# Optimization experiments

Measured on AMD Instinct MI355X. Metric: run time of the kernel, lower is better.

## Reference

```python
import jax, jax.numpy as jnp
import numpy as np

N, E, D, H = 50000, 800000, 256, 256
EPS = 1e-12


def _sage_pool(h, src, dst, W_pool, b_pool, W_self, W_neigh, b):
    # DGL SAGEConv aggregator_type='pool':
    #   m = relu(fc_pool(h_src)); h_neigh = max over in-neighbors; 
    #   out = fc_self(h_dst) + fc_neigh(h_neigh) + bias
    m = jax.nn.relu(h @ W_pool + b_pool)                # [N, D]
    msgs = m[src]                                        # [E, D] irregular gather
    agg = jax.ops.segment_max(msgs, dst, num_segments=N)  # [N, D]
    agg = jnp.where(jnp.isfinite(agg), agg, 0.0)         # zero-in-degree -> 0
    return h @ W_self + agg @ W_neigh + b


def _l2norm(h):
    # torch F.normalize(dim=1)
    n = jnp.linalg.norm(h, axis=1, keepdims=True)
    return h / jnp.maximum(n, EPS)


def setup_inputs() -> dict:
    key = jax.random.key(0)
    ks = jax.random.split(key, 13)
    s = 1.0 / np.sqrt(D)
    inp = {
        "x": jax.random.normal(ks[0], (N, D), jnp.float32),
        "src": jax.random.randint(ks[1], (E,), 0, N, jnp.int32),
        "dst": jax.random.randint(ks[2], (E,), 0, N, jnp.int32),
        "W_pool0": jax.random.normal(ks[3], (D, D), jnp.float32) * s,
        "b_pool0": jnp.zeros((D,), jnp.float32),
        "W_self0": jax.random.normal(ks[4], (D, H), jnp.float32) * s,
        "W_neigh0": jax.random.normal(ks[5], (D, H), jnp.float32) * s,
        "b0": jnp.zeros((H,), jnp.float32),
        "W_pool1": jax.random.normal(ks[6], (H, H), jnp.float32) * s,
        "b_pool1": jnp.zeros((H,), jnp.float32),
        "W_self1": jax.random.normal(ks[7], (H, H), jnp.float32) * s,
        "W_neigh1": jax.random.normal(ks[8], (H, H), jnp.float32) * s,
        "b1": jnp.zeros((H,), jnp.float32),
    }
    return inp


def reference(x, src, dst, W_pool0, b_pool0, W_self0, W_neigh0, b0,
              W_pool1, b_pool1, W_self1, W_neigh1, b1):
    # layer 0: conv -> relu -> l2-normalize -> dropout (identity at eval)
    h = _sage_pool(x, src, dst, W_pool0, b_pool0, W_self0, W_neigh0, b0)
    h = _l2norm(jax.nn.relu(h))
    enc_feat_input = h
    # layer 1 (last): conv only
    h = _sage_pool(h, src, dst, W_pool1, b_pool1, W_self1, W_neigh1, b1)
    return (h, enc_feat_input)
```

## Files before the change

### kernel.cpp

```cpp
#include <hip/hip_runtime.h>
#include <cstddef>

#define D256 256

typedef __attribute__((ext_vector_type(8))) short bf16x8;
typedef __attribute__((ext_vector_type(4))) float f32x4;

#define GLOAD16(gptr, lptr)                                                         \
    __builtin_amdgcn_global_load_lds(                                               \
        (const __attribute__((address_space(1))) unsigned int*)(gptr),              \
        (__attribute__((address_space(3))) unsigned int*)(lptr), 16, 0, 0)

__device__ __forceinline__ ushort f2bf(float f) {
    unsigned u = __float_as_uint(f);
    return (ushort)((u + 0x7FFFu + ((u >> 16) & 1u)) >> 16);
}
__device__ __forceinline__ ushort umax16(ushort a, ushort b) { return a > b ? a : b; }
__device__ __forceinline__ ushort4 vmax4(ushort4 a, ushort4 b) {
    return make_ushort4(umax16(a.x, b.x), umax16(a.y, b.y),
                        umax16(a.z, b.z), umax16(a.w, b.w));
}

template<int DUAL, int RELU, int OUT_BF16>
__global__ __launch_bounds__(256)
void mfma_gemm_kernel(const ushort* __restrict__ A, const ushort* __restrict__ Bt,
                      const ushort* __restrict__ A2, const ushort* __restrict__ Bt2,
                      const float* __restrict__ bias, void* __restrict__ outp, int M)
{
    constexpr int TILES = DUAL ? 4 : 2;
    constexpr int BUFSZ = TILES * 4096;
    __shared__ ushort smem[2 * BUFSZ];

    const int nwg  = gridDim.x;
    const int q    = nwg >> 3, r = nwg & 7;
    const int xcd  = blockIdx.x & 7, jj = blockIdx.x >> 3;
    const int wgid = (xcd < r ? xcd * (q + 1) : r * (q + 1) + (xcd - r) * q) + jj;

    const int t    = threadIdx.x;
    const int m0   = (wgid >> 1) * 128;
    const int n0   = (wgid & 1) * 128;
    const int lane = t & 63;
    const int wave = t >> 6;
    const int wr   = (wave >> 1) * 64;
    const int wc   = (wave & 1) * 64;
    const int lr   = lane & 15;
    const int kg   = lane >> 4;

    const int lrow  = lane >> 2;
    const int lch   = lane & 3;
    const int srow0 = wave * 32;

    f32x4 acc[4][4];
#pragma unroll
    for (int i = 0; i < 4; ++i)
#pragma unroll
        for (int j = 0; j < 4; ++j) acc[i][j] = (f32x4)(0.0f);

    auto STAGE = [&](int buf, int k0) {
        ushort* const base = smem + buf * BUFSZ;
#pragma unroll
        for (int i = 0; i < 2; ++i) {
            const int r2  = srow0 + i * 16;
            const int ar  = m0 + r2 + lrow;
            const int arc = ar < M ? ar : (M - 1);
            const size_t ga = (size_t)arc * D256 + k0 + lch * 8;
            const size_t gb = (size_t)(n0 + r2 + lrow) * D256 + k0 + lch * 8;
            GLOAD16(A + ga, base + r2 * 32);
            GLOAD16(Bt + gb, base + 4096 + r2 * 32);
            if (DUAL) {
                GLOAD16(A2 + ga, base + 8192 + r2 * 32);
                GLOAD16(Bt2 + gb, base + 12288 + r2 * 32);
            }
        }
    };

    STAGE(0, 0);
#pragma unroll
    for (int ks = 0; ks < 8; ++ks) {
        const int cur = ks & 1;
        __syncthreads();
        if (ks < 7) STAGE(cur ^ 1, (ks + 1) * 32);

        ushort* const base = smem + cur * BUFSZ;
        bf16x8 af[4], bf[4];
#pragma unroll
        for (int mi = 0; mi < 4; ++mi)
            af[mi] = *(const bf16x8*)&base[(wr + mi * 16 + lr) * 32 + kg * 8];
#pragma unroll
        for (int ni = 0; ni < 4; ++ni)
            bf[ni] = *(const bf16x8*)&base[4096 + (wc + ni * 16 + lr) * 32 + kg * 8];
#pragma unroll
        for (int mi = 0; mi < 4; ++mi)
#pragma unroll
            for (int ni = 0; ni < 4; ++ni)
                acc[mi][ni] = __builtin_amdgcn_mfma_f32_16x16x32_bf16(
                    bf[ni], af[mi], acc[mi][ni], 0, 0, 0);
        if (DUAL) {
            bf16x8 af2[4], bf2[4];
#pragma unroll
            for (int mi = 0; mi < 4; ++mi)
                af2[mi] = *(const bf16x8*)&base[8192 + (wr + mi * 16 + lr) * 32 + kg * 8];
#pragma unroll
            for (int ni = 0; ni < 4; ++ni)
                bf2[ni] = *(const bf16x8*)&base[12288 + (wc + ni * 16 + lr) * 32 + kg * 8];
#pragma unroll
            for (int mi = 0; mi < 4; ++mi)
#pragma unroll
                for (int ni = 0; ni < 4; ++ni)
                    acc[mi][ni] = __builtin_amdgcn_mfma_f32_16x16x32_bf16(
                        bf2[ni], af2[mi], acc[mi][ni], 0, 0, 0);
        }
    }

#pragma unroll
    for (int ni = 0; ni < 4; ++ni) {
        const int colb = n0 + wc + ni * 16 + kg * 4;
        const float4 bb = *(const float4*)(bias + colb);
#pragma unroll
        for (int mi = 0; mi < 4; ++mi) {
            const int row = m0 + wr + mi * 16 + lr;
            if (row < M) {
                const f32x4 a = acc[mi][ni];
                float4 o;
                o.x = a[0] + bb.x;
                o.y = a[1] + bb.y;
                o.z = a[2] + bb.z;
                o.w = a[3] + bb.w;
                if (RELU) {
                    o.x = fmaxf(o.x, 0.f); o.y = fmaxf(o.y, 0.f);
                    o.z = fmaxf(o.z, 0.f); o.w = fmaxf(o.w, 0.f);
                }
                if (OUT_BF16) {
                    ushort4 ob;
                    ob.x = f2bf(o.x); ob.y = f2bf(o.y);
                    ob.z = f2bf(o.z); ob.w = f2bf(o.w);
                    *(ushort4*)((ushort*)outp + (size_t)row * D256 + colb) = ob;
                } else {
                    *(float4*)((float*)outp + (size_t)row * D256 + colb) = o;
                }
            }
        }
    }
}

__global__ __launch_bounds__(256)
void f2bf_kernel(const float* __restrict__ in, ushort* __restrict__ out, int n4)
{
    const int i = blockIdx.x * 256 + threadIdx.x;
    if (i >= n4) return;
    const float4 v = ((const float4*)in)[i];
    ushort4 o;
    o.x = f2bf(v.x); o.y = f2bf(v.y); o.z = f2bf(v.z); o.w = f2bf(v.w);
    ((ushort4*)out)[i] = o;
}

struct WP  { const float* w; ushort* o; };
struct WP6 { WP p[6]; };
__global__ __launch_bounds__(256)
void wtrans_kernel(WP6 ps)
{
    const float* __restrict__ W = ps.p[blockIdx.z].w;
    ushort* __restrict__ O      = ps.p[blockIdx.z].o;
    __shared__ float sm[32][33];
    const int tx = threadIdx.x & 31, ty = threadIdx.x >> 5;
    const int k0 = blockIdx.x * 32, n0 = blockIdx.y * 32;
#pragma unroll
    for (int i = 0; i < 4; ++i)
        sm[ty + i * 8][tx] = W[(size_t)(k0 + ty + i * 8) * D256 + n0 + tx];
    __syncthreads();
#pragma unroll
    for (int i = 0; i < 4; ++i)
        O[(size_t)(n0 + ty + i * 8) * D256 + k0 + tx] = f2bf(sm[tx][ty + i * 8]);
}

__global__ __launch_bounds__(256)
void hist_kernel(const int* __restrict__ dst, int* __restrict__ deg, int E)
{
    const int nq = E >> 2;
    const int i  = blockIdx.x * 256 + threadIdx.x;
    if (i < nq) {
        const int4 d = ((const int4*)dst)[i];
        atomicAdd(&deg[d.x], 1);
        atomicAdd(&deg[d.y], 1);
        atomicAdd(&deg[d.z], 1);
        atomicAdd(&deg[d.w], 1);
    } else if (i == nq) {
        for (int e = nq * 4; e < E; ++e) atomicAdd(&deg[dst[e]], 1);
    }
}

__global__ __launch_bounds__(1024)
void blockscan_kernel(const int* __restrict__ deg, int* __restrict__ incl,
                      int* __restrict__ partials, int N)
{
    __shared__ int wt[16];
    const int i    = blockIdx.x * 1024 + threadIdx.x;
    const int lane = threadIdx.x & 63;
    const int wv   = threadIdx.x >> 6;
    const int v    = (i < N) ? deg[i] : 0;
    int s = v;
#pragma unroll
    for (int o = 1; o < 64; o <<= 1) {
        const int t = __shfl_up(s, o);
        if (lane >= o) s += t;
    }
    if (lane == 63) wt[wv] = s;
    __syncthreads();
    if (wv == 0 && lane < 16) {
        const int w = wt[lane];
        int ws = w;
#pragma unroll
        for (int o = 1; o < 16; o <<= 1) {
            const int t = __shfl_up(ws, o);
            if (lane >= o) ws += t;
        }
        wt[lane] = ws - w;
    }
    __syncthreads();
    s += wt[wv];
    if (i < N) incl[i] = s;
    if (threadIdx.x == 1023) partials[blockIdx.x] = s;
}

__global__ __launch_bounds__(1024)
void scanp_kernel(int* __restrict__ partials, int nb)
{
    __shared__ int sm[1024];
    const int v = (threadIdx.x < (unsigned)nb) ? partials[threadIdx.x] : 0;
    sm[threadIdx.x] = v;
    __syncthreads();
#pragma unroll
    for (int off = 1; off < 1024; off <<= 1) {
        const int t = (threadIdx.x >= (unsigned)off) ? sm[threadIdx.x - off] : 0;
        __syncthreads();
        sm[threadIdx.x] += t;
        __syncthreads();
    }
    if (threadIdx.x < (unsigned)nb) partials[threadIdx.x] = sm[threadIdx.x] - v;
}

__global__ __launch_bounds__(1024)
void finalize_kernel(const int* __restrict__ deg, const int* __restrict__ incl,
                     const int* __restrict__ partials, int* __restrict__ row_ptr,
                     int* __restrict__ cursor, int N, int E)
{
    const int i = blockIdx.x * 1024 + threadIdx.x;
    if (i < N) {
        const int ex = partials[blockIdx.x] + incl[i] - deg[i];
        row_ptr[i] = ex;
        cursor[i]  = ex;
    }
    if (i == 0) row_ptr[N] = E;
}

__global__ __launch_bounds__(256)
void bucket_kernel(const int* __restrict__ src, const int* __restrict__ dst,
                   int* __restrict__ cursor, int* __restrict__ esrc, int E)
{
    const int nq = E >> 2;
    const int i  = blockIdx.x * 256 + threadIdx.x;
    if (i < nq) {
        const int4 d = ((const int4*)dst)[i];
        const int4 s = ((const int4*)src)[i];
        esrc[atomicAdd(&cursor[d.x], 1)] = s.x;
        esrc[atomicAdd(&cursor[d.y], 1)] = s.y;
        esrc[atomicAdd(&cursor[d.z], 1)] = s.z;
        esrc[atomicAdd(&cursor[d.w], 1)] = s.w;
    } else if (i == nq) {
        for (int e = nq * 4; e < E; ++e)
            esrc[atomicAdd(&cursor[dst[e]], 1)] = src[e];
    }
}

__global__ __launch_bounds__(256)
void agg_max_kernel(const int* __restrict__ row_ptr, const int* __restrict__ esrc,
                    const ushort* __restrict__ m, ushort* __restrict__ agg, int N)
{
    const int wid  = (int)(((size_t)blockIdx.x * 256 + threadIdx.x) >> 6);
    const int lane = threadIdx.x & 63;
    if (wid >= N) return;
    const int beg = row_ptr[wid];
    const int end = row_ptr[wid + 1];
    const size_t off = (size_t)(lane * 4);

    ushort4 a0 = make_ushort4(0, 0, 0, 0);
    ushort4 a1 = a0, a2 = a0, a3 = a0;
    int e = beg;
    for (; e + 8 <= end; e += 8) {
        int s[8];
#pragma unroll
        for (int q = 0; q < 8; ++q) s[q] = esrc[e + q];
        ushort4 v[8];
#pragma unroll
        for (int q = 0; q < 8; ++q)
            v[q] = *(const ushort4*)(m + (size_t)s[q] * D256 + off);
        a0 = vmax4(a0, vmax4(v[0], v[4]));
        a1 = vmax4(a1, vmax4(v[1], v[5]));
        a2 = vmax4(a2, vmax4(v[2], v[6]));
        a3 = vmax4(a3, vmax4(v[3], v[7]));
    }
    for (; e + 2 <= end; e += 2) {
        const int s0 = esrc[e];
        const int s1 = esrc[e + 1];
        const ushort4 v0 = *(const ushort4*)(m + (size_t)s0 * D256 + off);
        const ushort4 v1 = *(const ushort4*)(m + (size_t)s1 * D256 + off);
        a0 = vmax4(a0, v0);
        a1 = vmax4(a1, v1);
    }
    if (e < end) {
        const ushort4 v0 = *(const ushort4*)(m + (size_t)esrc[e] * D256 + off);
        a2 = vmax4(a2, v0);
    }
    const ushort4 r = vmax4(vmax4(a0, a1), vmax4(a2, a3));
    *(ushort4*)(agg + (size_t)wid * D256 + off) = r;
}

__global__ __launch_bounds__(256)
void l2norm_kernel(const float* __restrict__ in, float* __restrict__ out_f,
                   ushort* __restrict__ out_b, int M)
{
    const int wid  = (int)(((size_t)blockIdx.x * 256 + threadIdx.x) >> 6);
    const int lane = threadIdx.x & 63;
    if (wid >= M) return;
    const float4 v = *(const float4*)(in + (size_t)wid * D256 + lane * 4);
    float ss = v.x * v.x + v.y * v.y + v.z * v.z + v.w * v.w;
#pragma unroll
    for (int o = 32; o >= 1; o >>= 1) ss += __shfl_xor(ss, o);
    const float inv = 1.0f / fmaxf(sqrtf(ss), 1e-12f);
    float4 o4;
    o4.x = v.x * inv; o4.y = v.y * inv; o4.z = v.z * inv; o4.w = v.w * inv;
    *(float4*)(out_f + (size_t)wid * D256 + lane * 4) = o4;
    ushort4 ob;
    ob.x = f2bf(o4.x); ob.y = f2bf(o4.y); ob.z = f2bf(o4.z); ob.w = f2bf(o4.w);
    *(ushort4*)(out_b + (size_t)wid * D256 + lane * 4) = ob;
}

extern "C" void kernel_launch(void* const* d_in, const int* in_sizes, int n_in,
                              void* d_out, int out_size, void* d_ws, size_t ws_size,
                              hipStream_t stream)
{
    const float* x        = (const float*)d_in[0];
    const int*   src      = (const int*)  d_in[1];
    const int*   dst      = (const int*)  d_in[2];
    const float* W_pool0  = (const float*)d_in[3];
    const float* b_pool0  = (const float*)d_in[4];
    const float* W_self0  = (const float*)d_in[5];
    const float* W_neigh0 = (const float*)d_in[6];
    const float* b0       = (const float*)d_in[7];
    const float* W_pool1  = (const float*)d_in[8];
    const float* b_pool1  = (const float*)d_in[9];
    const float* W_self1  = (const float*)d_in[10];
    const float* W_neigh1 = (const float*)d_in[11];
    const float* b1       = (const float*)d_in[12];

    const int N = in_sizes[0] / D256;
    const int E = in_sizes[1];
    const size_t NR = (size_t)N * D256;

    float* h1  = (float*)d_out;
    float* enc = (float*)d_out + NR;

    ushort* xb   = (ushort*)d_ws;
    ushort* mb   = xb + NR;
    ushort* aggb = mb + NR;
    float*  tmp  = (float*)(aggb + NR);
    ushort* Bt   = (ushort*)(tmp + NR);
    int* row_ptr = (int*)(Bt + 6 * 256 * 256);
    int* cursor  = row_ptr + (N + 1);
    int* deg     = cursor + N;
    int* incl    = deg + N;
    int* partials= incl + N;
    int* esrc    = partials + 1024;

    ushort* Bt_pool0  = Bt + 0 * 65536;
    ushort* Bt_self0  = Bt + 1 * 65536;
    ushort* Bt_neigh0 = Bt + 2 * 65536;
    ushort* Bt_pool1  = Bt + 3 * 65536;
    ushort* Bt_self1  = Bt + 4 * 65536;
    ushort* Bt_neigh1 = Bt + 5 * 65536;

    const int  gemm_blocks = ((N + 127) / 128) * 2;
    const int  q_blocks    = ((E >> 2) + 1 + 255) / 256;
    const int  node_blocks = (N + 3) / 4;
    const int  conv_blocks = (int)((NR / 4 + 255) / 256);
    const int  scan_blocks = (N + 1023) / 1024;

    WP6 wp;
    wp.p[0] = { W_pool0,  Bt_pool0  };
    wp.p[1] = { W_self0,  Bt_self0  };
    wp.p[2] = { W_neigh0, Bt_neigh0 };
    wp.p[3] = { W_pool1,  Bt_pool1  };
    wp.p[4] = { W_self1,  Bt_self1  };
    wp.p[5] = { W_neigh1, Bt_neigh1 };
    wtrans_kernel<<<dim3(8, 8, 6), 256, 0, stream>>>(wp);
    f2bf_kernel<<<conv_blocks, 256, 0, stream>>>(x, xb, (int)(NR / 4));

    hipMemsetAsync(deg, 0, (size_t)N * sizeof(int), stream);
    hist_kernel<<<q_blocks, 256, 0, stream>>>(dst, deg, E);
    blockscan_kernel<<<scan_blocks, 1024, 0, stream>>>(deg, incl, partials, N);
    scanp_kernel<<<1, 1024, 0, stream>>>(partials, scan_blocks);
    finalize_kernel<<<scan_blocks, 1024, 0, stream>>>(deg, incl, partials,
                                                      row_ptr, cursor, N, E);
    bucket_kernel<<<q_blocks, 256, 0, stream>>>(src, dst, cursor, esrc, E);

    mfma_gemm_kernel<0,1,1><<<gemm_blocks, 256, 0, stream>>>(xb, Bt_pool0, nullptr, nullptr,
                                                             b_pool0, mb, N);
    agg_max_kernel<<<node_blocks, 256, 0, stream>>>(row_ptr, esrc, mb, aggb, N);
    mfma_gemm_kernel<1,1,0><<<gemm_blocks, 256, 0, stream>>>(xb, Bt_self0, aggb, Bt_neigh0,
                                                             b0, tmp, N);
    l2norm_kernel<<<node_blocks, 256, 0, stream>>>(tmp, enc, xb, N);

    mfma_gemm_kernel<0,1,1><<<gemm_blocks, 256, 0, stream>>>(xb, Bt_pool1, nullptr, nullptr,
                                                             b_pool1, mb, N);
    agg_max_kernel<<<node_blocks, 256, 0, stream>>>(row_ptr, esrc, mb, aggb, N);
    mfma_gemm_kernel<1,0,0><<<gemm_blocks, 256, 0, stream>>>(xb, Bt_self1, aggb, Bt_neigh1,
                                                             b1, h1, N);
}
```

Baseline: 357.4 us.

## Fuse layer-0 dual GEMM with ReLU and L2 normalization epilogue

After: 355.4 us. Within noise of the previous version (-0.6%).

```diff
diff --git a/kernel.cpp b/kernel.cpp
--- a/kernel.cpp
+++ b/kernel.cpp
@@ -144,6 +144,129 @@
 }
 
 __global__ __launch_bounds__(256)
+void mfma_dual_l2n_kernel(const ushort* A, const ushort* __restrict__ Bt,
+                          const ushort* __restrict__ A2, const ushort* __restrict__ Bt2,
+                          const float* __restrict__ bias,
+                          float* __restrict__ enc_f, ushort* enc_b, int M)
+{
+    __shared__ ushort smem[24576];
+    __shared__ float  ssq_lds[128][2];
+
+    const int t    = threadIdx.x;
+    const int m0   = blockIdx.x * 128;
+    const int lane = t & 63;
+    const int wave = t >> 6;
+    const int wr   = (wave >> 1) * 64;
+    const int wc   = (wave & 1) * 128;
+    const int lr   = lane & 15;
+    const int kg   = lane >> 4;
+    const int lrow = lane >> 2;
+    const int lch  = lane & 3;
+
+    f32x4 acc[4][8];
+#pragma unroll
+    for (int i = 0; i < 4; ++i)
+#pragma unroll
+        for (int j = 0; j < 8; ++j) acc[i][j] = (f32x4)(0.0f);
+
+    for (int ks = 0; ks < 8; ++ks) {
+        const int k0 = ks * 32;
+        __syncthreads();
+#pragma unroll
+        for (int i = 0; i < 2; ++i) {
+            const int r2  = wave * 32 + i * 16;
+            const int ar  = m0 + r2 + lrow;
+            const int arc = ar < M ? ar : (M - 1);
+            const size_t ga = (size_t)arc * D256 + k0 + lch * 8;
+            GLOAD16(A + ga, smem + r2 * 32);
+            GLOAD16(A2 + ga, smem + 12288 + r2 * 32);
+        }
+#pragma unroll
+        for (int i = 0; i < 4; ++i) {
+            const int r2 = wave * 64 + i * 16;
+            const size_t gb = (size_t)(r2 + lrow) * D256 + k0 + lch * 8;
+            GLOAD16(Bt + gb, smem + 4096 + r2 * 32);
+            GLOAD16(Bt2 + gb, smem + 16384 + r2 * 32);
+        }
+        __syncthreads();
+
+        bf16x8 af[4];
+#pragma unroll
+        for (int mi = 0; mi < 4; ++mi)
+            af[mi] = *(const bf16x8*)&smem[(wr + mi * 16 + lr) * 32 + kg * 8];
+#pragma unroll
+        for (int ni = 0; ni < 8; ++ni) {
+            const bf16x8 b = *(const bf16x8*)&smem[4096 + (wc + ni * 16 + lr) * 32 + kg * 8];
+#pragma unroll
+            for (int mi = 0; mi < 4; ++mi)
+                acc[mi][ni] = __builtin_amdgcn_mfma_f32_16x16x32_bf16(
+                    b, af[mi], acc[mi][ni], 0, 0, 0);
+        }
+#pragma unroll
+        for (int mi = 0; mi < 4; ++mi)
+            af[mi] = *(const bf16x8*)&smem[12288 + (wr + mi * 16 + lr) * 32 + kg * 8];
+#pragma unroll
+        for (int ni = 0; ni < 8; ++ni) {
+            const bf16x8 b = *(const bf16x8*)&smem[16384 + (wc + ni * 16 + lr) * 32 + kg * 8];
+#pragma unroll
+            for (int mi = 0; mi < 4; ++mi)
+                acc[mi][ni] = __builtin_amdgcn_mfma_f32_16x16x32_bf16(
+                    b, af[mi], acc[mi][ni], 0, 0, 0);
+        }
+    }
+
+    float ssq[4] = {0.f, 0.f, 0.f, 0.f};
+#pragma unroll
+    for (int mi = 0; mi < 4; ++mi)
+#pragma unroll
+        for (int ni = 0; ni < 8; ++ni) {
+            const int colb = wc + ni * 16 + kg * 4;
+            const float4 bb = *(const float4*)(bias + colb);
+            f32x4 a = acc[mi][ni];
+            a[0] = fmaxf(a[0] + bb.x, 0.f);
+            a[1] = fmaxf(a[1] + bb.y, 0.f);
+            a[2] = fmaxf(a[2] + bb.z, 0.f);
+            a[3] = fmaxf(a[3] + bb.w, 0.f);
+            acc[mi][ni] = a;
+            ssq[mi] += a[0] * a[0] + a[1] * a[1] + a[2] * a[2] + a[3] * a[3];
+        }
+#pragma unroll
+    for (int mi = 0; mi < 4; ++mi) {
+        ssq[mi] += __shfl_xor(ssq[mi], 16);
+        ssq[mi] += __shfl_xor(ssq[mi], 32);
+    }
+    __syncthreads();
+    if (kg == 0) {
+#pragma unroll
+        for (int mi = 0; mi < 4; ++mi)
+            ssq_lds[wr + mi * 16 + lr][wave & 1] = ssq[mi];
+    }
+    __syncthreads();
+#pragma unroll
+    for (int mi = 0; mi < 4; ++mi) {
+        const int rrow = wr + mi * 16 + lr;
+        const int row  = m0 + rrow;
+        const float tot = ssq_lds[rrow][0] + ssq_lds[rrow][1];
+        const float inv = 1.0f / fmaxf(sqrtf(tot), 1e-12f);
+        if (row < M) {
+#pragma unroll
+            for (int ni = 0; ni < 8; ++ni) {
+                const int colb = wc + ni * 16 + kg * 4;
+                const f32x4 a = acc[mi][ni];
+                float4 o;
+                o.x = a[0] * inv; o.y = a[1] * inv;
+                o.z = a[2] * inv; o.w = a[3] * inv;
+                *(float4*)(enc_f + (size_t)row * D256 + colb) = o;
+                ushort4 ob;
+                ob.x = f2bf(o.x); ob.y = f2bf(o.y);
+                ob.z = f2bf(o.z); ob.w = f2bf(o.w);
+                *(ushort4*)(enc_b + (size_t)row * D256 + colb) = ob;
+            }
+        }
+    }
+}
+
+__global__ __launch_bounds__(256)
 void f2bf_kernel(const float* __restrict__ in, ushort* __restrict__ out, int n4)
 {
     const int i = blockIdx.x * 256 + threadIdx.x;
@@ -313,26 +436,6 @@
     }
     const ushort4 r = vmax4(vmax4(a0, a1), vmax4(a2, a3));
     *(ushort4*)(agg + (size_t)wid * D256 + off) = r;
-}
-
-__global__ __launch_bounds__(256)
-void l2norm_kernel(const float* __restrict__ in, float* __restrict__ out_f,
-                   ushort* __restrict__ out_b, int M)
-{
-    const int wid  = (int)(((size_t)blockIdx.x * 256 + threadIdx.x) >> 6);
-    const int lane = threadIdx.x & 63;
-    if (wid >= M) return;
-    const float4 v = *(const float4*)(in + (size_t)wid * D256 + lane * 4);
-    float ss = v.x * v.x + v.y * v.y + v.z * v.z + v.w * v.w;
-#pragma unroll
-    for (int o = 32; o >= 1; o >>= 1) ss += __shfl_xor(ss, o);
-    const float inv = 1.0f / fmaxf(sqrtf(ss), 1e-12f);
-    float4 o4;
-    o4.x = v.x * inv; o4.y = v.y * inv; o4.z = v.z * inv; o4.w = v.w * inv;
-    *(float4*)(out_f + (size_t)wid * D256 + lane * 4) = o4;
-    ushort4 ob;
-    ob.x = f2bf(o4.x); ob.y = f2bf(o4.y); ob.z = f2bf(o4.z); ob.w = f2bf(o4.w);
-    *(ushort4*)(out_b + (size_t)wid * D256 + lane * 4) = ob;
 }
 
 extern "C" void kernel_launch(void* const* d_in, const int* in_sizes, int n_in,
@@ -380,6 +483,7 @@
     ushort* Bt_neigh1 = Bt + 5 * 65536;
 
     const int  gemm_blocks = ((N + 127) / 128) * 2;
+    const int  l2n_blocks  = (N + 127) / 128;
     const int  q_blocks    = ((E >> 2) + 1 + 255) / 256;
     const int  node_blocks = (N + 3) / 4;
     const int  conv_blocks = (int)((NR / 4 + 255) / 256);
@@ -406,9 +510,8 @@
     mfma_gemm_kernel<0,1,1><<<gemm_blocks, 256, 0, stream>>>(xb, Bt_pool0, nullptr, nullptr,
                                                              b_pool0, mb, N);
     agg_max_kernel<<<node_blocks, 256, 0, stream>>>(row_ptr, esrc, mb, aggb, N);
-    mfma_gemm_kernel<1,1,0><<<gemm_blocks, 256, 0, stream>>>(xb, Bt_self0, aggb, Bt_neigh0,
-                                                             b0, tmp, N);
-    l2norm_kernel<<<node_blocks, 256, 0, stream>>>(tmp, enc, xb, N);
+    mfma_dual_l2n_kernel<<<l2n_blocks, 256, 0, stream>>>(xb, Bt_self0, aggb, Bt_neigh0,
+                                                         b0, enc, xb, N);
 
     mfma_gemm_kernel<0,1,1><<<gemm_blocks, 256, 0, stream>>>(xb, Bt_pool1, nullptr, nullptr,
                                                              b_pool1, mb, N);
```
